# Kernel optimization log

Hardware: AMD Instinct MI355X
Metric: run time of the kernel (lower is better)

The kernel has to match this reference:

```python
import jax, jax.numpy as jnp
import numpy as np

N, L, E = 8, 512, 128
H_DIM = 256            # hidden_dim
Q_DIM = 512            # query_vec dim (config.input_dim, q_update=False)
IN_DIM = 2 * H_DIM     # mean_max tok2ent doubles dim
N_HEADS, N_TYPE = 4, 3
FH = H_DIM // N_HEADS  # per-head out_dim = 64
LSTM_IN, LSTM_H = 2 * H_DIM, H_DIM // 2  # 512 -> 128 per direction
LRELU = 0.2


def lstm_dir(x, Wih, Whh, bih, bhh, reverse):
    # x: (N, L, D); PyTorch gate order i, f, g, o
    if reverse:
        x = jnp.flip(x, axis=1)
    n = x.shape[0]
    def step(carry, xt):
        h, c = carry
        gates = xt @ Wih.T + h @ Whh.T + bih + bhh
        i, f, g, o = jnp.split(gates, 4, axis=-1)
        c = jax.nn.sigmoid(f) * c + jax.nn.sigmoid(i) * jnp.tanh(g)
        h = jax.nn.sigmoid(o) * jnp.tanh(c)
        return (h, c), h
    init = (jnp.zeros((n, LSTM_H), x.dtype), jnp.zeros((n, LSTM_H), x.dtype))
    _, ys = jax.lax.scan(step, init, jnp.swapaxes(x, 0, 1))
    ys = jnp.swapaxes(ys, 0, 1)
    if reverse:
        ys = jnp.flip(ys, axis=1)
    return ys


def setup_inputs():
    key = jax.random.key(0)
    ks = jax.random.split(key, 16)
    s = 0.05
    return {
        'doc_state': jax.random.normal(ks[0], (N, L, H_DIM), jnp.float32),
        'query_vec': jax.random.normal(ks[1], (N, Q_DIM), jnp.float32),
        'context_mask': jnp.ones((N, L), jnp.float32),
        'ent_mapping': (jax.random.uniform(ks[2], (N, E, L)) < 0.03).astype(jnp.float32),
        'ent_mask': jnp.ones((N, E), jnp.float32),
        'query_weight': jax.random.normal(ks[3], (Q_DIM, IN_DIM), jnp.float32) * s,
        'W_type': jax.random.normal(ks[4], (N_HEADS, N_TYPE, IN_DIM, FH), jnp.float32) * s,
        'a_type': jax.random.normal(ks[5], (N_HEADS, N_TYPE, 2 * FH, 1), jnp.float32) * s,
        'qattn_W1': jax.random.normal(ks[6], (N_HEADS, N_TYPE, Q_DIM, 2 * FH), jnp.float32) * s,
        'qattn_W2': jax.random.normal(ks[7], (N_HEADS, N_TYPE, 2 * FH, 2 * FH), jnp.float32) * s,
        'Wih_f': jax.random.normal(ks[8], (4 * LSTM_H, LSTM_IN), jnp.float32) * s,
        'Whh_f': jax.random.normal(ks[9], (4 * LSTM_H, LSTM_H), jnp.float32) * s,
        'bih_f': jnp.zeros((4 * LSTM_H,), jnp.float32),
        'bhh_f': jnp.zeros((4 * LSTM_H,), jnp.float32),
        'Wih_b': jax.random.normal(ks[10], (4 * LSTM_H, LSTM_IN), jnp.float32) * s,
        'Whh_b': jax.random.normal(ks[11], (4 * LSTM_H, LSTM_H), jnp.float32) * s,
        'bih_b': jnp.zeros((4 * LSTM_H,), jnp.float32),
        'bhh_b': jnp.zeros((4 * LSTM_H,), jnp.float32),
        'context_lens': jnp.full((N,), L, jnp.int32),
        'graphs': jax.random.randint(ks[12], (N, E, E), 0, N_TYPE + 1, jnp.int32),
    }


def reference(doc_state, query_vec, context_mask, ent_mapping, ent_mask,
              query_weight, W_type, a_type, qattn_W1, qattn_W2,
              Wih_f, Whh_f, bih_f, bhh_f, Wih_b, Whh_b, bih_b, bhh_b,
              context_lens, graphs):
    adj = graphs  # (N, E, E), values in {0..N_TYPE}
    # --- MeanMaxPooling tok2ent (entity_lens computed as in BasicBlock) ---
    ent_len = ent_mapping.sum(-1)
    ent_len = ent_len + (ent_len == 0)
    es = ent_mapping[:, :, :, None] * doc_state[:, None]          # (N,E,L,d)
    max_p = es.max(axis=2)
    mean_p = es.sum(axis=2) / ent_len[:, :, None]
    entity_state = jnp.concatenate([max_p, mean_p], axis=-1)      # (N,E,2d)
    # --- query-conditioned soft mask ---
    temp = np.float32(np.sqrt(Q_DIM * IN_DIM))
    query = query_vec @ query_weight                              # (N,2d)
    query_scores = jnp.einsum('ned,nd->ne', entity_state, query)[..., None] / temp
    softmask = query_scores * ent_mask[:, :, None]                # (N,E,1)
    adj_mask = jax.nn.sigmoid(softmask)
    # --- multi-head multi-relation GAT (score computed without E^2*2d concat) ---
    h_all = jnp.einsum('ned,htdf->htnef', entity_state, W_type)   # (H,T,N,E,f)
    qg = jax.nn.relu(jnp.einsum('nd,htdg->htng', query_vec, qattn_W1))
    qg = jax.nn.sigmoid(jnp.einsum('htng,htgk->htnk', qg, qattn_W2))  # (H,T,N,2f)
    g1, g2 = qg[..., :FH], qg[..., FH:]
    a = a_type[..., 0]                                            # (H,T,2f)
    a1, a2 = a[..., :FH], a[..., FH:]
    src = jnp.einsum('htnef,htnf,htf->htne', h_all, g1, a1)
    dst = jnp.einsum('htnef,htnf,htf->htne', h_all, g2, a2)
    sc = src[..., :, None] + dst[..., None, :]                    # (H,T,N,E,E)
    sc = jnp.where(sc > 0, sc, LRELU * sc)                        # lrelu:0.2
    type_ids = jnp.arange(1, N_TYPE + 1, dtype=adj.dtype).reshape(1, N_TYPE, 1, 1, 1)
    scores = jnp.sum(jnp.where(adj[None, None] == type_ids, sc, jnp.float32(0)), axis=1)  # (H,N,E,E)
    scores = jnp.where(adj[None] > 0, scores, jnp.float32(-1e30))
    coefs = jax.nn.softmax(scores, axis=-1)
    # original code multiplies the LAST edge-type's h by node_mask, then aggregates
    h_last = h_all[:, -1] * adj_mask[None]                        # (H,N,E,f)
    heads = jnp.einsum('hnij,hnjf->hnif', coefs, h_last)          # (H,N,E,f)
    ent_out = jnp.transpose(heads, (1, 2, 0, 3)).reshape(N, E, H_DIM)
    entity_state2 = jax.nn.relu(ent_out)                          # (N,E,hid)
    # --- InteractionLayer (LSTM branch; all lengths == L so packing is a no-op) ---
    expand = jnp.einsum('ned,nel->nld', entity_state2, ent_mapping)  # (N,L,hid)
    inp = jnp.concatenate([expand, doc_state], axis=-1)           # (N,L,2*hid)
    fwd = lstm_dir(inp, Wih_f, Whh_f, bih_f, bhh_f, False)
    bwd = lstm_dir(inp, Wih_b, Whh_b, bih_b, bhh_b, True)
    doc_out = jnp.concatenate([fwd, bwd], axis=-1)                # (N,L,hid)
    return doc_out, entity_state2, softmask
```

## Files before the change

### kernel.cpp

```cpp
#include <hip/hip_runtime.h>
#include <math.h>

typedef _Float16 h2 __attribute__((ext_vector_type(2)));
typedef _Float16 f16x8 __attribute__((ext_vector_type(8)));
typedef __attribute__((ext_vector_type(8))) short bf16x8;
typedef __attribute__((ext_vector_type(4))) float f32x4;

__device__ __forceinline__ float sigm(float x){ return 1.f/(1.f+expf(-x)); }

__device__ __forceinline__ float fsigm(float x){
  float e = __expf(-x);
  return __builtin_amdgcn_rcpf(1.f + e);
}
__device__ __forceinline__ float ftanh(float x){
  float xx = fminf(fmaxf(x, -15.f), 15.f);
  float e = __expf(2.f * xx);
  return 1.f - 2.f * __builtin_amdgcn_rcpf(e + 1.f);
}
__device__ __forceinline__ h2 u2h(unsigned u){
  union { unsigned u; h2 h; } x; x.u = u; return x.h;
}
template<int CTRL>
__device__ __forceinline__ float qperm(float v){
  return __int_as_float(__builtin_amdgcn_mov_dpp(__float_as_int(v), CTRL, 0xf, 0xf, true));
}
__device__ __forceinline__ unsigned short f2bf(float f){
  union{float f; unsigned u;} x; x.f = f;
  unsigned r = x.u + 0x7FFF + ((x.u >> 16) & 1);
  return (unsigned short)(r >> 16);
}

__global__ void k_ent_state(const float* __restrict__ doc, const float* __restrict__ emap,
                            float* __restrict__ ES, _Float16* __restrict__ ES16){
  int ne = blockIdx.x;
  int n = ne >> 7;
  int tid = threadIdx.x;
  __shared__ int idx_l[512];
  __shared__ int cnt_s;
  if (tid < 64){
    int total = 0;
    for (int base = 0; base < 512; base += 64){
      float m = emap[(size_t)ne*512 + base + tid];
      unsigned long long mask = __ballot(m != 0.f);
      int pos = __popcll(mask & ((1ull << tid) - 1ull));
      if (m != 0.f) idx_l[total + pos] = base + tid;
      total += __popcll(mask);
    }
    if (tid == 0) cnt_s = total;
  }
  __syncthreads();
  int cnt = cnt_s;
  const float* dbase = doc + (size_t)n*512*256 + tid;
  const float* mrow = emap + (size_t)ne*512;
  float sum = 0.f, mx = -3.402823e38f, msum = 0.f;
  for (int i = 0; i < cnt; i++){
    int l = idx_l[i];
    float m = mrow[l];
    float v = m * dbase[(size_t)l*256];
    sum += v; mx = fmaxf(mx, v); msum += m;
  }
  if (cnt < 512) mx = fmaxf(mx, 0.f);
  float elen = (msum == 0.f) ? 1.f : msum;
  float mean = sum / elen;
  float* o = ES + (size_t)ne*512;
  o[tid] = mx;
  o[256 + tid] = mean;
  _Float16* o16 = ES16 + (size_t)ne*512;
  o16[tid] = (_Float16)mx;
  o16[256 + tid] = (_Float16)mean;
}

__global__ __launch_bounds__(256) void k_wtprep(const float* __restrict__ Wt,
                                                _Float16* __restrict__ WtT){
  int kt = blockIdx.x;
  int ht = blockIdx.y;
  int tid = threadIdx.x;
  __shared__ _Float16 tile[64][65];
  for (int rep = 0; rep < 16; rep++){
    int linear = rep*256 + tid;
    int k = linear >> 6, f = linear & 63;
    tile[f][k] = (_Float16)Wt[((size_t)ht*512 + kt*64 + k)*64 + f];
  }
  __syncthreads();
  for (int rep = 0; rep < 16; rep++){
    int linear = rep*256 + tid;
    int f = linear >> 6, k = linear & 63;
    WtT[((size_t)ht*64 + f)*512 + kt*64 + k] = tile[f][k];
  }
}

__global__ __launch_bounds__(256) void k_colidx(const float* __restrict__ emap,
                                                int* __restrict__ cidx, int* __restrict__ ccnt){
  int lt = blockIdx.x;
  int n = blockIdx.y;
  int l0 = lt*32;
  int tid = threadIdx.x;
  __shared__ float tile[128][33];
  int l = tid & 31, eg = tid >> 5;
  for (int i = 0; i < 16; i++){
    int e = eg*16 + i;
    tile[e][l] = emap[((size_t)n*128 + e)*512 + l0 + l];
  }
  __syncthreads();
  if (tid < 32){
    int ll = tid;
    int b = n*512 + l0 + ll;
    int* out = cidx + (size_t)b*128;
    int cnt = 0;
    for (int e = 0; e < 128; e++){
      if (tile[e][ll] != 0.f) out[cnt++] = e;
    }
    ccnt[b] = cnt;
  }
}

__global__ __launch_bounds__(256) void k_query2(const float* __restrict__ qv,
                                                const float* __restrict__ qw,
                                                float* __restrict__ Q){
  int b = blockIdx.x;
  int n = b >> 3, ct = b & 7;
  int tid = threadIdx.x;
  int col = ct*64 + (tid & 63), ks = tid >> 6;
  const float* qvp = qv + n*512 + ks*128;
  const float* qwp = qw + (size_t)(ks*128)*512 + col;
  float acc = 0.f;
  for (int k = 0; k < 128; k++) acc += qvp[k] * qwp[(size_t)k*512];
  __shared__ float part[4][64];
  part[ks][tid & 63] = acc;
  __syncthreads();
  if (tid < 64)
    Q[n*512 + ct*64 + tid] = part[0][tid] + part[1][tid] + part[2][tid] + part[3][tid];
}

__global__ __launch_bounds__(64) void k_qscore2(const float* __restrict__ ES,
                         const float* __restrict__ Q, const float* __restrict__ emask,
                         float* __restrict__ sm_out, float* __restrict__ AM){
  int ne = blockIdx.x;
  int n = ne >> 7;
  int lane = threadIdx.x;
  const float* es = ES + (size_t)ne*512;
  const float* q = Q + n*512;
  float a = 0.f;
  for (int k = lane; k < 512; k += 64) a += es[k] * q[k];
  #pragma unroll
  for (int o = 32; o > 0; o >>= 1) a += __shfl_xor(a, o, 64);
  if (lane == 0){
    float s = (a * (1.f/512.f)) * emask[ne];
    sm_out[ne] = s;
    AM[ne] = sigm(s);
  }
}

__global__ __launch_bounds__(256) void k_hall(const _Float16* __restrict__ ES16,
                                              const _Float16* __restrict__ WtT,
                                              float* __restrict__ HALL){
  int net = blockIdx.x;
  int ht  = blockIdx.y;
  int tid = threadIdx.x;
  int lane = tid & 63, w = tid >> 6;
  int wm = w >> 1, wg = w & 1;
  int m0 = net*64 + wm*32;
  int f0 = wg*32;
  int lr = lane & 15, lk8 = (lane >> 4) * 8;

  const _Float16* a0p = ES16 + (size_t)(m0 + lr)*512 + lk8;
  const _Float16* a1p = a0p + (size_t)16*512;
  const _Float16* b0p = WtT + ((size_t)ht*64 + f0 + lr)*512 + lk8;
  const _Float16* b1p = b0p + (size_t)16*512;

  f32x4 acc[2][2] = {};
  for (int k0 = 0; k0 < 512; k0 += 32){
    f16x8 af[2], bfr[2];
    af[0] = *(const f16x8*)a0p;
    af[1] = *(const f16x8*)a1p;
    bfr[0] = *(const f16x8*)b0p;
    bfr[1] = *(const f16x8*)b1p;
    a0p += 32; a1p += 32; b0p += 32; b1p += 32;
    #pragma unroll
    for (int im = 0; im < 2; im++)
      #pragma unroll
      for (int ig = 0; ig < 2; ig++)
        acc[im][ig] = __builtin_amdgcn_mfma_f32_16x16x32_f16(af[im], bfr[ig], acc[im][ig], 0, 0, 0);
  }
  int crow = (lane >> 4) * 4;
  int ccol = lane & 15;
  #pragma unroll
  for (int im = 0; im < 2; im++)
    #pragma unroll
    for (int ig = 0; ig < 2; ig++){
      int f = f0 + ig*16 + ccol;
      #pragma unroll
      for (int r = 0; r < 4; r++){
        int m = m0 + im*16 + crow + r;
        HALL[((size_t)ht*1024 + m)*64 + f] = acc[im][ig][r];
      }
    }
}

__global__ __launch_bounds__(256) void k_qattn(const float* __restrict__ qv,
                        const float* __restrict__ W1, const float* __restrict__ W2,
                        const float* __restrict__ at, float* __restrict__ WSRC,
                        float* __restrict__ WDST){
  int b = blockIdx.x;
  int ht = b >> 3, n = b & 7;
  int tid = threadIdx.x;
  int f = tid & 127, kh = tid >> 7;
  __shared__ float qv_s[512];
  __shared__ float part[2][128];
  __shared__ float qg1[128];
  for (int i = tid; i < 512; i += 256) qv_s[i] = qv[n*512 + i];
  __syncthreads();
  const float* w1 = W1 + (size_t)ht*512*128 + (size_t)kh*256*128 + f;
  float acc = 0.f;
  for (int k = 0; k < 256; k++) acc += qv_s[kh*256 + k] * w1[(size_t)k*128];
  part[kh][f] = acc;
  __syncthreads();
  if (kh == 0) qg1[f] = fmaxf(part[0][f] + part[1][f], 0.f);
  __syncthreads();
  const float* w2 = W2 + (size_t)ht*128*128 + (size_t)kh*64*128 + f;
  float acc2 = 0.f;
  for (int g = 0; g < 64; g++) acc2 += qg1[kh*64 + g] * w2[(size_t)g*128];
  part[kh][f] = acc2;
  __syncthreads();
  if (kh == 0){
    float coef = sigm(part[0][f] + part[1][f]) * at[ht*128 + f];
    if (f < 64) WSRC[(ht*8 + n)*64 + f] = coef;
    else        WDST[(ht*8 + n)*64 + f - 64] = coef;
  }
}

__global__ void k_srcdst(const float* __restrict__ HALL, const float* __restrict__ WSRC,
                         const float* __restrict__ WDST, float* __restrict__ SRC,
                         float* __restrict__ DST){
  int b = blockIdx.x;
  int e = threadIdx.x;
  __shared__ float w1[64], w2[64];
  if (e < 64) w1[e] = WSRC[b*64 + e]; else w2[e-64] = WDST[b*64 + e - 64];
  __syncthreads();
  int ht = b >> 3, n = b & 7;
  const float* h = HALL + ((size_t)ht*1024 + n*128 + e)*64;
  float s = 0.f, d = 0.f;
  #pragma unroll 8
  for (int f = 0; f < 64; f++){ float hv = h[f]; s += hv*w1[f]; d += hv*w2[f]; }
  SRC[b*128 + e] = s; DST[b*128 + e] = d;
}

__global__ void k_attn(const float* __restrict__ HALL, const float* __restrict__ SRC,
                       const float* __restrict__ DST, const float* __restrict__ AM,
                       const int* __restrict__ adj, float* __restrict__ ES2,
                       float* __restrict__ out_ent){
  int b = blockIdx.x;
  int h = b >> 6, n = (b >> 3) & 7, chunk = b & 7;
  int i0 = chunk*16;
  int tid = threadIdx.x;
  __shared__ float dst_l[3][128];
  __shared__ float src_l[3][16];
  __shared__ float hl[128][65];
  __shared__ float coef_l[128];
  __shared__ float redbuf[2];
  __shared__ float part2[2][64];
  for (int idx = tid; idx < 384; idx += 128){
    int t = idx >> 7, j = idx & 127;
    dst_l[t][j] = DST[((h*3 + t)*8 + n)*128 + j];
  }
  if (tid < 48){
    int t = tid >> 4, r = tid & 15;
    src_l[t][r] = SRC[((h*3 + t)*8 + n)*128 + i0 + r];
  }
  for (int idx = tid; idx < 8192; idx += 128){
    int j = idx >> 6, f = idx & 63;
    hl[j][f] = HALL[((size_t)(h*3 + 2)*1024 + n*128 + j)*64 + f] * AM[n*128 + j];
  }
  __syncthreads();
  const int* arow = adj + (size_t)n*128*128;
  int w = tid >> 6, f = tid & 63;
  for (int r = 0; r < 16; r++){
    int i = i0 + r;
    int a = arow[(size_t)i*128 + tid];
    float s;
    if (a > 0){
      float v = src_l[a-1][r] + dst_l[a-1][tid];
      s = v > 0.f ? v : 0.2f*v;
    } else s = -1e30f;
    float m = s;
    #pragma unroll
    for (int o = 32; o > 0; o >>= 1) m = fmaxf(m, __shfl_xor(m, o, 64));
    if ((tid & 63) == 0) redbuf[w] = m;
    __syncthreads();
    float mx = fmaxf(redbuf[0], redbuf[1]);
    float p = expf(s - mx);
    float ps = p;
    #pragma unroll
    for (int o = 32; o > 0; o >>= 1) ps += __shfl_xor(ps, o, 64);
    __syncthreads();
    if ((tid & 63) == 0) redbuf[w] = ps;
    __syncthreads();
    float denom = redbuf[0] + redbuf[1];
    coef_l[tid] = p / denom;
    __syncthreads();
    float acc = 0.f;
    for (int jj = 0; jj < 64; jj++) acc += coef_l[w*64 + jj] * hl[w*64 + jj][f];
    part2[w][f] = acc;
    __syncthreads();
    if (tid < 64){
      float v = fmaxf(part2[0][tid] + part2[1][tid], 0.f);
      size_t oidx = ((size_t)n*128 + i)*256 + h*64 + tid;
      ES2[oidx] = v;
      out_ent[oidx] = v;
    }
    __syncthreads();
  }
}

__global__ void k_expand(const float* __restrict__ ES2, const float* __restrict__ emap,
                         const float* __restrict__ doc, const int* __restrict__ cidx,
                         const int* __restrict__ ccnt, float* __restrict__ INP){
  int b = blockIdx.x;
  int n = b >> 9, l = b & 511;
  int tid = threadIdx.x;
  int cnt = ccnt[b];
  const int* idx = cidx + (size_t)b*128;
  float acc = 0.f;
  const float* e2 = ES2 + (size_t)n*128*256 + tid;
  for (int i = 0; i < cnt; i++){
    int e = idx[i];
    float m = emap[((size_t)n*128 + e)*512 + l];
    acc += m * e2[(size_t)e*256];
  }
  float* o = INP + (size_t)b*512;
  o[tid] = acc;
  o[256 + tid] = doc[(size_t)b*256 + tid];
}

__global__ __launch_bounds__(256) void k_gatein(const float* __restrict__ INP,
                         const float* __restrict__ Wf, const float* __restrict__ Wb,
                         const float* __restrict__ bihf, const float* __restrict__ bhhf,
                         const float* __restrict__ bihb, const float* __restrict__ bhhb,
                         float* __restrict__ GF, float* __restrict__ GB){
  int mt = blockIdx.x, gt = blockIdx.y, dir = blockIdx.z;
  const float* W = dir ? Wb : Wf;
  float* Gout = dir ? GB : GF;
  const float* bi = dir ? bihb : bihf;
  const float* bh = dir ? bhhb : bhhf;
  int tid = threadIdx.x;
  int lane = tid & 63, w = tid >> 6;
  int wm = w >> 1, wg = w & 1;
  int m0 = mt*64 + wm*32;
  int g0 = gt*64 + wg*32;
  int lr = lane & 15, lk8 = (lane >> 4) * 8;

  const float* a0p = INP + (size_t)(m0 + lr)*512 + lk8;
  const float* a1p = a0p + (size_t)16*512;
  const float* b0p = W   + (size_t)(g0 + lr)*512 + lk8;
  const float* b1p = b0p + (size_t)16*512;

  f32x4 acc[2][2] = {};
  for (int k0 = 0; k0 < 512; k0 += 32){
    bf16x8 af[2], bfr[2];
    {
      float4 u = *(const float4*)a0p, v = *(const float4*)(a0p + 4);
      bf16x8 r; r[0]=(short)f2bf(u.x); r[1]=(short)f2bf(u.y); r[2]=(short)f2bf(u.z); r[3]=(short)f2bf(u.w);
      r[4]=(short)f2bf(v.x); r[5]=(short)f2bf(v.y); r[6]=(short)f2bf(v.z); r[7]=(short)f2bf(v.w);
      af[0]=r;
    }
    {
      float4 u = *(const float4*)a1p, v = *(const float4*)(a1p + 4);
      bf16x8 r; r[0]=(short)f2bf(u.x); r[1]=(short)f2bf(u.y); r[2]=(short)f2bf(u.z); r[3]=(short)f2bf(u.w);
      r[4]=(short)f2bf(v.x); r[5]=(short)f2bf(v.y); r[6]=(short)f2bf(v.z); r[7]=(short)f2bf(v.w);
      af[1]=r;
    }
    {
      float4 u = *(const float4*)b0p, v = *(const float4*)(b0p + 4);
      bf16x8 r; r[0]=(short)f2bf(u.x); r[1]=(short)f2bf(u.y); r[2]=(short)f2bf(u.z); r[3]=(short)f2bf(u.w);
      r[4]=(short)f2bf(v.x); r[5]=(short)f2bf(v.y); r[6]=(short)f2bf(v.z); r[7]=(short)f2bf(v.w);
      bfr[0]=r;
    }
    {
      float4 u = *(const float4*)b1p, v = *(const float4*)(b1p + 4);
      bf16x8 r; r[0]=(short)f2bf(u.x); r[1]=(short)f2bf(u.y); r[2]=(short)f2bf(u.z); r[3]=(short)f2bf(u.w);
      r[4]=(short)f2bf(v.x); r[5]=(short)f2bf(v.y); r[6]=(short)f2bf(v.z); r[7]=(short)f2bf(v.w);
      bfr[1]=r;
    }
    a0p += 32; a1p += 32; b0p += 32; b1p += 32;
    #pragma unroll
    for (int im = 0; im < 2; im++)
      #pragma unroll
      for (int ig = 0; ig < 2; ig++)
        acc[im][ig] = __builtin_amdgcn_mfma_f32_16x16x32_bf16(af[im], bfr[ig], acc[im][ig], 0, 0, 0);
  }
  int crow = (lane >> 4) * 4;
  int ccol = lane & 15;
  #pragma unroll
  for (int im = 0; im < 2; im++)
    #pragma unroll
    for (int ig = 0; ig < 2; ig++){
      int g = g0 + ig*16 + ccol;
      float bias = bi[g] + bh[g];
      int p = (g & 127)*4 + (g >> 7);
      #pragma unroll
      for (int r = 0; r < 4; r++){
        int m = m0 + im*16 + crow + r;
        Gout[(size_t)m*512 + p] = acc[im][ig][r] + bias;
      }
    }
}

__global__ __launch_bounds__(256) void k_lstm(const float* __restrict__ GF,
                                              const float* __restrict__ GB,
                                              const float* __restrict__ Whhf,
                                              const float* __restrict__ Whhb,
                                              float* __restrict__ out){
  int b = blockIdx.x;
  int dir = b >> 3, n = b & 7;
  const float* G = dir ? GB : GF;
  const float* Whh = dir ? Whhb : Whhf;
  int tid = threadIdx.x;
  int j = tid >> 1;
  int s = tid & 1;

  h2 wreg[4][32];
  #pragma unroll
  for (int q = 0; q < 4; q++){
    const float* wp = Whh + (size_t)(q*128 + j)*128 + 64*s;
    #pragma unroll
    for (int kk = 0; kk < 32; kk++){
      h2 p; p[0] = (_Float16)wp[2*kk]; p[1] = (_Float16)wp[2*kk+1];
      wreg[q][kk] = p;
    }
  }

  __shared__ __align__(16) _Float16 h_l[2][128];
  if (tid < 128) h_l[0][tid] = (_Float16)0.f;

  const float4* Gp = (const float4*)(G + (size_t)n*512*512) + (dir ? (size_t)511*128 : 0) + j;
  const int gstep = dir ? -128 : 128;
  float* outp = out + (size_t)n*512*256 + (dir ? (size_t)511*256 : 0) + dir*128 + j;
  const int ostep = dir ? -256 : 256;

  float4 ga, gb, gc, gd;
  ga = *Gp; Gp += gstep;
  gb = *Gp; Gp += gstep;
  gc = *Gp; Gp += gstep;
  gd = *Gp; Gp += gstep;
  float c = 0.f;
  __syncthreads();

#define LSTM_STEP(RB, GREG)                                                    \
  {                                                                            \
    const uint4* hb = (const uint4*)(&h_l[RB][64*s]);                          \
    uint4 hv[8];                                                               \
    _Pragma("unroll")                                                          \
    for (int r = 0; r < 8; r++) hv[r] = hb[r];                                 \
    float gci = GREG.x, gcf = GREG.y, gcg = GREG.z, gco = GREG.w;              \
    GREG = *Gp; Gp += gstep;                                                   \
    float accf[4];                                                             \
    _Pragma("unroll")                                                          \
    for (int q = 0; q < 4; q++){                                               \
      h2 a0; a0[0]=(_Float16)0.f; a0[1]=(_Float16)0.f; h2 a1 = a0;             \
      _Pragma("unroll")                                                        \
      for (int r = 0; r < 8; r++){                                             \
        a0 += wreg[q][4*r+0] * u2h(hv[r].x);                                   \
        a1 += wreg[q][4*r+1] * u2h(hv[r].y);                                   \
        a0 += wreg[q][4*r+2] * u2h(hv[r].z);                                   \
        a1 += wreg[q][4*r+3] * u2h(hv[r].w);                                   \
      }                                                                        \
      h2 hs = a0 + a1;                                                         \
      accf[q] = (float)hs[0] + (float)hs[1];                                   \
    }                                                                          \
    _Pragma("unroll")                                                          \
    for (int q = 0; q < 4; q++){                                               \
      accf[q] += qperm<0xB1>(accf[q]);                                         \
    }                                                                          \
    float vi = accf[0] + gci, vf = accf[1] + gcf;                              \
    float vg = accf[2] + gcg, vo = accf[3] + gco;                              \
    c = fsigm(vf) * c + fsigm(vi) * ftanh(vg);                                 \
    float hval = fsigm(vo) * ftanh(c);                                         \
    if (s == 0) h_l[RB^1][j] = (_Float16)hval;                                 \
    else        *outp = hval;                                                  \
    outp += ostep;                                                             \
    asm volatile("s_waitcnt lgkmcnt(0)\n\ts_barrier" ::: "memory");            \
  }

  for (int t = 0; t < 512; t += 4){
    LSTM_STEP(0, ga)
    LSTM_STEP(1, gb)
    LSTM_STEP(0, gc)
    LSTM_STEP(1, gd)
  }
#undef LSTM_STEP
}

extern "C" void kernel_launch(void* const* d_in, const int* in_sizes, int n_in,
                              void* d_out, int out_size, void* d_ws, size_t ws_size,
                              hipStream_t stream){
  const float* doc   = (const float*)d_in[0];
  const float* qvec  = (const float*)d_in[1];
  const float* emap  = (const float*)d_in[3];
  const float* emask = (const float*)d_in[4];
  const float* qw    = (const float*)d_in[5];
  const float* Wt    = (const float*)d_in[6];
  const float* at    = (const float*)d_in[7];
  const float* qa1   = (const float*)d_in[8];
  const float* qa2   = (const float*)d_in[9];
  const float* Wihf  = (const float*)d_in[10];
  const float* Whhf  = (const float*)d_in[11];
  const float* bihf  = (const float*)d_in[12];
  const float* bhhf  = (const float*)d_in[13];
  const float* Wihb  = (const float*)d_in[14];
  const float* Whhb  = (const float*)d_in[15];
  const float* bihb  = (const float*)d_in[16];
  const float* bhhb  = (const float*)d_in[17];
  const int*   adj   = (const int*)d_in[19];

  float* out = (float*)d_out;
  float* out_doc = out;
  float* out_ent = out + 8*512*256;
  float* out_sm  = out_ent + 8*128*256;

  float* w = (float*)d_ws;
  float* ES   = w; w += 8*128*512;
  float* AM   = w; w += 8*128;
  float* Q    = w; w += 8*512;
  float* HALL = w; w += 12*1024*64;
  float* WSRC = w; w += 12*8*64;
  float* WDST = w; w += 12*8*64;
  float* SRC  = w; w += 12*8*128;
  float* DST  = w; w += 12*8*128;
  float* ES2  = w; w += 8*128*256;
  float* INP  = w; w += 8*512*512;
  float* GF   = w; w += 8*512*512;
  w += 4096;
  float* GB   = w; w += 8*512*512;
  w += 4096;
  _Float16* ES16 = (_Float16*)w; w += 8*128*512/2;
  _Float16* WtT  = (_Float16*)w; w += 12*64*512/2;
  int* cidx = (int*)w; w += 4096*128;
  int* ccnt = (int*)w; w += 4096;

  hipLaunchKernelGGL(k_colidx,    dim3(16,8), dim3(256), 0, stream, emap, cidx, ccnt);
  hipLaunchKernelGGL(k_wtprep,    dim3(8,12), dim3(256), 0, stream, Wt, WtT);
  hipLaunchKernelGGL(k_ent_state, dim3(1024), dim3(256), 0, stream, doc, emap, ES, ES16);
  hipLaunchKernelGGL(k_query2,    dim3(64),   dim3(256), 0, stream, qvec, qw, Q);
  hipLaunchKernelGGL(k_qscore2,   dim3(1024), dim3(64),  0, stream, ES, Q, emask, out_sm, AM);
  hipLaunchKernelGGL(k_hall,      dim3(16,12),dim3(256), 0, stream, ES16, WtT, HALL);
  hipLaunchKernelGGL(k_qattn,     dim3(96),   dim3(256), 0, stream, qvec, qa1, qa2, at, WSRC, WDST);
  hipLaunchKernelGGL(k_srcdst,    dim3(96),   dim3(128), 0, stream, HALL, WSRC, WDST, SRC, DST);
  hipLaunchKernelGGL(k_attn,      dim3(256),  dim3(128), 0, stream, HALL, SRC, DST, AM, adj, ES2, out_ent);
  hipLaunchKernelGGL(k_expand,    dim3(4096), dim3(256), 0, stream, ES2, emap, doc, cidx, ccnt, INP);
  hipLaunchKernelGGL(k_gatein,    dim3(64,8,2), dim3(256), 0, stream, INP, Wihf, Wihb, bihf, bhhf, bihb, bhhb, GF, GB);
  hipLaunchKernelGGL(k_lstm,      dim3(16),   dim3(256), 0, stream, GF, GB, Whhf, Whhb, out_doc);
}
```

Before: 421.0 us.

## Batch LSTM recurrence across sequences with MFMA in one block per direction

The recurrent LSTM kernel changes from one block per (direction, batch) doing packed-half dot products to one 512-thread block per direction. That block computes the hidden-to-gate product for all 8 sequences at once with 16x16x32 f16 MFMA instructions, padding the batch to 16 columns. A new prep kernel writes Whh into fp16 in MFMA A-fragment layout so the weights load straight into registers. This cuts per-step ALU work but puts each direction on a single CU and wastes half the MFMA columns on padding. Latency per step now depends on the MFMA chain plus the transcendental math.

```diff
diff --git a/kernel.cpp b/kernel.cpp
--- a/kernel.cpp
+++ b/kernel.cpp
@@ -16,13 +16,6 @@
   float xx = fminf(fmaxf(x, -15.f), 15.f);
   float e = __expf(2.f * xx);
   return 1.f - 2.f * __builtin_amdgcn_rcpf(e + 1.f);
-}
-__device__ __forceinline__ h2 u2h(unsigned u){
-  union { unsigned u; h2 h; } x; x.u = u; return x.h;
-}
-template<int CTRL>
-__device__ __forceinline__ float qperm(float v){
-  return __int_as_float(__builtin_amdgcn_mov_dpp(__float_as_int(v), CTRL, 0xf, 0xf, true));
 }
 __device__ __forceinline__ unsigned short f2bf(float f){
   union{float f; unsigned u;} x; x.f = f;
@@ -89,6 +82,25 @@
   }
 }
 
+__global__ __launch_bounds__(256) void k_whhprep(const float* __restrict__ Whhf,
+                                                 const float* __restrict__ Whhb,
+                                                 _Float16* __restrict__ WA){
+  int dir = blockIdx.y;
+  const float* Whh = dir ? Whhb : Whhf;
+  _Float16* outb = WA + (size_t)dir*512*128;
+  int slot = blockIdx.x*256 + threadIdx.x;
+  int l = slot & 63;
+  int tile = slot >> 6;
+  int kc = tile & 3, mt = (tile >> 2) & 3, wv = tile >> 4;
+  int lane_lo = l & 15, khi = l >> 4;
+  int girow = wv*64 + mt*16 + lane_lo;
+  int j = girow >> 2, q = girow & 3;
+  const float* src = Whh + (size_t)(q*128 + j)*128 + kc*32 + khi*8;
+  _Float16* dst = outb + (size_t)slot*8;
+  #pragma unroll
+  for (int i = 0; i < 8; i++) dst[i] = (_Float16)src[i];
+}
+
 __global__ __launch_bounds__(256) void k_colidx(const float* __restrict__ emap,
                                                 int* __restrict__ cidx, int* __restrict__ ccnt){
   int lt = blockIdx.x;
@@ -105,10 +117,10 @@
   if (tid < 32){
     int ll = tid;
     int b = n*512 + l0 + ll;
-    int* out = cidx + (size_t)b*128;
+    int* outp = cidx + (size_t)b*128;
     int cnt = 0;
     for (int e = 0; e < 128; e++){
-      if (tile[e][ll] != 0.f) out[cnt++] = e;
+      if (tile[e][ll] != 0.f) outp[cnt++] = e;
     }
     ccnt[b] = cnt;
   }
@@ -405,87 +417,85 @@
     }
 }
 
-__global__ __launch_bounds__(256) void k_lstm(const float* __restrict__ GF,
+__global__ __launch_bounds__(512) void k_lstm(const float* __restrict__ GF,
                                               const float* __restrict__ GB,
-                                              const float* __restrict__ Whhf,
-                                              const float* __restrict__ Whhb,
+                                              const _Float16* __restrict__ WA,
                                               float* __restrict__ out){
-  int b = blockIdx.x;
-  int dir = b >> 3, n = b & 7;
+  int dir = blockIdx.x;
   const float* G = dir ? GB : GF;
-  const float* Whh = dir ? Whhb : Whhf;
-  int tid = threadIdx.x;
-  int j = tid >> 1;
-  int s = tid & 1;
-
-  h2 wreg[4][32];
-  #pragma unroll
-  for (int q = 0; q < 4; q++){
-    const float* wp = Whh + (size_t)(q*128 + j)*128 + 64*s;
-    #pragma unroll
-    for (int kk = 0; kk < 32; kk++){
-      h2 p; p[0] = (_Float16)wp[2*kk]; p[1] = (_Float16)wp[2*kk+1];
-      wreg[q][kk] = p;
-    }
-  }
-
-  __shared__ __align__(16) _Float16 h_l[2][128];
-  if (tid < 128) h_l[0][tid] = (_Float16)0.f;
-
-  const float4* Gp = (const float4*)(G + (size_t)n*512*512) + (dir ? (size_t)511*128 : 0) + j;
-  const int gstep = dir ? -128 : 128;
-  float* outp = out + (size_t)n*512*256 + (dir ? (size_t)511*256 : 0) + dir*128 + j;
-  const int ostep = dir ? -256 : 256;
-
-  float4 ga, gb, gc, gd;
-  ga = *Gp; Gp += gstep;
-  gb = *Gp; Gp += gstep;
-  gc = *Gp; Gp += gstep;
-  gd = *Gp; Gp += gstep;
-  float c = 0.f;
+  const _Float16* wa = WA + (size_t)dir*512*128;
+  int tid = threadIdx.x;
+  int lane = tid & 63, wv = tid >> 6;
+  int n = lane & 15;
+  int nc = n & 7;
+  int uhi = lane >> 4;
+  bool active = (n < 8);
+
+  f16x8 afrag[4][4];
+  #pragma unroll
+  for (int mt = 0; mt < 4; mt++)
+    #pragma unroll
+    for (int kc = 0; kc < 4; kc++){
+      int slot = ((wv*4 + mt)*4 + kc)*64 + lane;
+      afrag[mt][kc] = *(const f16x8*)(wa + (size_t)slot*8);
+    }
+
+  __shared__ __align__(16) _Float16 h_lds[2][16][136];
+  for (int i = tid; i < 2*16*136; i += 512) ((_Float16*)h_lds)[i] = (_Float16)0.f;
+
+  int j0 = 16*wv + uhi;
+  int tt0 = dir ? 511 : 0;
+  const float* Gp = G + (size_t)(nc*512 + tt0)*512 + 4*j0;
+  const long gstep = dir ? -512 : 512;
+  float* outp = out + (size_t)(nc*512 + tt0)*256 + dir*128 + j0;
+  const long ostep = dir ? -256 : 256;
+
+  float4 gA[4], gB[4];
+  #pragma unroll
+  for (int mt = 0; mt < 4; mt++) gA[mt] = *(const float4*)(Gp + mt*16);
+  Gp += gstep;
+  #pragma unroll
+  for (int mt = 0; mt < 4; mt++) gB[mt] = *(const float4*)(Gp + mt*16);
+  Gp += gstep;
+
+  float cst[4] = {0.f, 0.f, 0.f, 0.f};
   __syncthreads();
 
 #define LSTM_STEP(RB, GREG)                                                    \
   {                                                                            \
-    const uint4* hb = (const uint4*)(&h_l[RB][64*s]);                          \
-    uint4 hv[8];                                                               \
+    const _Float16* hrow = &h_lds[RB][n][0];                                   \
+    f16x8 bfrag[4];                                                            \
     _Pragma("unroll")                                                          \
-    for (int r = 0; r < 8; r++) hv[r] = hb[r];                                 \
-    float gci = GREG.x, gcf = GREG.y, gcg = GREG.z, gco = GREG.w;              \
-    GREG = *Gp; Gp += gstep;                                                   \
-    float accf[4];                                                             \
+    for (int kc = 0; kc < 4; kc++)                                             \
+      bfrag[kc] = *(const f16x8*)(hrow + kc*32 + uhi*8);                       \
+    f32x4 acc[4] = {};                                                         \
     _Pragma("unroll")                                                          \
-    for (int q = 0; q < 4; q++){                                               \
-      h2 a0; a0[0]=(_Float16)0.f; a0[1]=(_Float16)0.f; h2 a1 = a0;             \
+    for (int mt = 0; mt < 4; mt++)                                             \
       _Pragma("unroll")                                                        \
-      for (int r = 0; r < 8; r++){                                             \
-        a0 += wreg[q][4*r+0] * u2h(hv[r].x);                                   \
-        a1 += wreg[q][4*r+1] * u2h(hv[r].y);                                   \
-        a0 += wreg[q][4*r+2] * u2h(hv[r].z);                                   \
-        a1 += wreg[q][4*r+3] * u2h(hv[r].w);                                   \
+      for (int kc = 0; kc < 4; kc++)                                           \
+        acc[mt] = __builtin_amdgcn_mfma_f32_16x16x32_f16(afrag[mt][kc],        \
+                      bfrag[kc], acc[mt], 0, 0, 0);                            \
+    _Pragma("unroll")                                                          \
+    for (int mt = 0; mt < 4; mt++){                                            \
+      float4 g = GREG[mt];                                                     \
+      GREG[mt] = *(const float4*)(Gp + mt*16);                                 \
+      float vi = acc[mt][0] + g.x, vf = acc[mt][1] + g.y;                      \
+      float vg = acc[mt][2] + g.z, vo = acc[mt][3] + g.w;                      \
+      cst[mt] = fsigm(vf)*cst[mt] + fsigm(vi)*ftanh(vg);                       \
+      float hval = fsigm(vo)*ftanh(cst[mt]);                                   \
+      if (active){                                                             \
+        h_lds[RB^1][n][j0 + 4*mt] = (_Float16)hval;                            \
+        outp[4*mt] = hval;                                                     \
       }                                                                        \
-      h2 hs = a0 + a1;                                                         \
-      accf[q] = (float)hs[0] + (float)hs[1];                                   \
     }                                                                          \
-    _Pragma("unroll")                                                          \
-    for (int q = 0; q < 4; q++){                                               \
-      accf[q] += qperm<0xB1>(accf[q]);                                         \
-    }                                                                          \
-    float vi = accf[0] + gci, vf = accf[1] + gcf;                              \
-    float vg = accf[2] + gcg, vo = accf[3] + gco;                              \
-    c = fsigm(vf) * c + fsigm(vi) * ftanh(vg);                                 \
-    float hval = fsigm(vo) * ftanh(c);                                         \
-    if (s == 0) h_l[RB^1][j] = (_Float16)hval;                                 \
-    else        *outp = hval;                                                  \
+    Gp += gstep;                                                               \
     outp += ostep;                                                             \
     asm volatile("s_waitcnt lgkmcnt(0)\n\ts_barrier" ::: "memory");            \
   }
 
-  for (int t = 0; t < 512; t += 4){
-    LSTM_STEP(0, ga)
-    LSTM_STEP(1, gb)
-    LSTM_STEP(0, gc)
-    LSTM_STEP(1, gd)
+  for (int t = 0; t < 512; t += 2){
+    LSTM_STEP(0, gA)
+    LSTM_STEP(1, gB)
   }
 #undef LSTM_STEP
 }
@@ -534,11 +544,13 @@
   w += 4096;
   _Float16* ES16 = (_Float16*)w; w += 8*128*512/2;
   _Float16* WtT  = (_Float16*)w; w += 12*64*512/2;
+  _Float16* WA   = (_Float16*)w; w += 2*512*128/2;
   int* cidx = (int*)w; w += 4096*128;
   int* ccnt = (int*)w; w += 4096;
 
   hipLaunchKernelGGL(k_colidx,    dim3(16,8), dim3(256), 0, stream, emap, cidx, ccnt);
   hipLaunchKernelGGL(k_wtprep,    dim3(8,12), dim3(256), 0, stream, Wt, WtT);
+  hipLaunchKernelGGL(k_whhprep,   dim3(32,2), dim3(256), 0, stream, Whhf, Whhb, WA);
   hipLaunchKernelGGL(k_ent_state, dim3(1024), dim3(256), 0, stream, doc, emap, ES, ES16);
   hipLaunchKernelGGL(k_query2,    dim3(64),   dim3(256), 0, stream, qvec, qw, Q);
   hipLaunchKernelGGL(k_qscore2,   dim3(1024), dim3(64),  0, stream, ES, Q, emask, out_sm, AM);
@@ -548,5 +560,5 @@
   hipLaunchKernelGGL(k_attn,      dim3(256),  dim3(128), 0, stream, HALL, SRC, DST, AM, adj, ES2, out_ent);
   hipLaunchKernelGGL(k_expand,    dim3(4096), dim3(256), 0, stream, ES2, emap, doc, cidx, ccnt, INP);
   hipLaunchKernelGGL(k_gatein,    dim3(64,8,2), dim3(256), 0, stream, INP, Wihf, Wihb, bihf, bhhf, bihb, bhhb, GF, GB);
-  hipLaunchKernelGGL(k_lstm,      dim3(16),   dim3(256), 0, stream, GF, GB, Whhf, Whhb, out_doc);
-}
+  hipLaunchKernelGGL(k_lstm,      dim3(2),    dim3(512), 0, stream, GF, GB, WA, out_doc);
+}
```

Measured after the change: 699.5 us. 1.66x slower.

## Merge independent prologue kernels into two block-dispatched megakernels

Applied to the files above, without the earlier changes.

Combines colidx, wtprep, ent_state, query and qattn into one kernel that picks its role from the block index, and combines qscore and the HALL MFMA GEMM into a second one. Qscore now packs four entities per 256-thread block. This cuts launches from twelve to seven and lets independent work run concurrently, aiming to remove launch gaps and tail idle time. The cost is a larger shared-memory footprint and register allocation set by the heaviest branch, which may lower occupancy for the lighter roles.

```diff
diff --git a/kernel.cpp b/kernel.cpp
--- a/kernel.cpp
+++ b/kernel.cpp
@@ -30,202 +30,195 @@
   return (unsigned short)(r >> 16);
 }
 
-__global__ void k_ent_state(const float* __restrict__ doc, const float* __restrict__ emap,
-                            float* __restrict__ ES, _Float16* __restrict__ ES16){
-  int ne = blockIdx.x;
-  int n = ne >> 7;
+__global__ __launch_bounds__(256) void k_mega1(
+    const float* __restrict__ doc, const float* __restrict__ emap,
+    const float* __restrict__ qv, const float* __restrict__ qw,
+    const float* __restrict__ Wt, const float* __restrict__ W1,
+    const float* __restrict__ W2, const float* __restrict__ at,
+    int* __restrict__ cidx, int* __restrict__ ccnt,
+    _Float16* __restrict__ WtT, float* __restrict__ ES,
+    _Float16* __restrict__ ES16, float* __restrict__ Q,
+    float* __restrict__ WSRC, float* __restrict__ WDST){
+  __shared__ __align__(16) char smem[16896];
+  int b = blockIdx.x;
   int tid = threadIdx.x;
-  __shared__ int idx_l[512];
-  __shared__ int cnt_s;
-  if (tid < 64){
-    int total = 0;
-    for (int base = 0; base < 512; base += 64){
-      float m = emap[(size_t)ne*512 + base + tid];
-      unsigned long long mask = __ballot(m != 0.f);
-      int pos = __popcll(mask & ((1ull << tid) - 1ull));
-      if (m != 0.f) idx_l[total + pos] = base + tid;
-      total += __popcll(mask);
-    }
-    if (tid == 0) cnt_s = total;
-  }
-  __syncthreads();
-  int cnt = cnt_s;
-  const float* dbase = doc + (size_t)n*512*256 + tid;
-  const float* mrow = emap + (size_t)ne*512;
-  float sum = 0.f, mx = -3.402823e38f, msum = 0.f;
-  for (int i = 0; i < cnt; i++){
-    int l = idx_l[i];
-    float m = mrow[l];
-    float v = m * dbase[(size_t)l*256];
-    sum += v; mx = fmaxf(mx, v); msum += m;
-  }
-  if (cnt < 512) mx = fmaxf(mx, 0.f);
-  float elen = (msum == 0.f) ? 1.f : msum;
-  float mean = sum / elen;
-  float* o = ES + (size_t)ne*512;
-  o[tid] = mx;
-  o[256 + tid] = mean;
-  _Float16* o16 = ES16 + (size_t)ne*512;
-  o16[tid] = (_Float16)mx;
-  o16[256 + tid] = (_Float16)mean;
-}
-
-__global__ __launch_bounds__(256) void k_wtprep(const float* __restrict__ Wt,
-                                                _Float16* __restrict__ WtT){
-  int kt = blockIdx.x;
-  int ht = blockIdx.y;
+
+  if (b < 128){
+    float (*tile)[33] = (float(*)[33])smem;
+    int lt = b & 15, n = b >> 4;
+    int l0 = lt*32;
+    int l = tid & 31, eg = tid >> 5;
+    for (int i = 0; i < 16; i++){
+      int e = eg*16 + i;
+      tile[e][l] = emap[((size_t)n*128 + e)*512 + l0 + l];
+    }
+    __syncthreads();
+    if (tid < 32){
+      int ll = tid;
+      int bb = n*512 + l0 + ll;
+      int* outp = cidx + (size_t)bb*128;
+      int cnt = 0;
+      for (int e = 0; e < 128; e++){
+        if (tile[e][ll] != 0.f) outp[cnt++] = e;
+      }
+      ccnt[bb] = cnt;
+    }
+  } else if (b < 224){
+    _Float16 (*tile)[65] = (_Float16(*)[65])smem;
+    int rb = b - 128;
+    int kt = rb & 7, ht = rb >> 3;
+    for (int rep = 0; rep < 16; rep++){
+      int linear = rep*256 + tid;
+      int k = linear >> 6, f = linear & 63;
+      tile[f][k] = (_Float16)Wt[((size_t)ht*512 + kt*64 + k)*64 + f];
+    }
+    __syncthreads();
+    for (int rep = 0; rep < 16; rep++){
+      int linear = rep*256 + tid;
+      int f = linear >> 6, k = linear & 63;
+      WtT[((size_t)ht*64 + f)*512 + kt*64 + k] = tile[f][k];
+    }
+  } else if (b < 1248){
+    int* idx_l = (int*)smem;
+    int* cnt_p = (int*)(smem + 2048);
+    int ne = b - 224;
+    int n = ne >> 7;
+    if (tid < 64){
+      int total = 0;
+      for (int base = 0; base < 512; base += 64){
+        float m = emap[(size_t)ne*512 + base + tid];
+        unsigned long long mask = __ballot(m != 0.f);
+        int pos = __popcll(mask & ((1ull << tid) - 1ull));
+        if (m != 0.f) idx_l[total + pos] = base + tid;
+        total += __popcll(mask);
+      }
+      if (tid == 0) *cnt_p = total;
+    }
+    __syncthreads();
+    int cnt = *cnt_p;
+    const float* dbase = doc + (size_t)n*512*256 + tid;
+    const float* mrow = emap + (size_t)ne*512;
+    float sum = 0.f, mx = -3.402823e38f, msum = 0.f;
+    for (int i = 0; i < cnt; i++){
+      int l = idx_l[i];
+      float m = mrow[l];
+      float v = m * dbase[(size_t)l*256];
+      sum += v; mx = fmaxf(mx, v); msum += m;
+    }
+    if (cnt < 512) mx = fmaxf(mx, 0.f);
+    float elen = (msum == 0.f) ? 1.f : msum;
+    float mean = sum / elen;
+    float* o = ES + (size_t)ne*512;
+    o[tid] = mx;
+    o[256 + tid] = mean;
+    _Float16* o16 = ES16 + (size_t)ne*512;
+    o16[tid] = (_Float16)mx;
+    o16[256 + tid] = (_Float16)mean;
+  } else if (b < 1312){
+    float (*part)[64] = (float(*)[64])smem;
+    int rb = b - 1248;
+    int n = rb >> 3, ct = rb & 7;
+    int col = ct*64 + (tid & 63), ks = tid >> 6;
+    const float* qvp = qv + n*512 + ks*128;
+    const float* qwp = qw + (size_t)(ks*128)*512 + col;
+    float acc = 0.f;
+    for (int k = 0; k < 128; k++) acc += qvp[k] * qwp[(size_t)k*512];
+    part[ks][tid & 63] = acc;
+    __syncthreads();
+    if (tid < 64)
+      Q[n*512 + ct*64 + tid] = part[0][tid] + part[1][tid] + part[2][tid] + part[3][tid];
+  } else {
+    float* qv_s = (float*)smem;
+    float* partb = qv_s + 512;
+    float* qg1 = partb + 256;
+    int rb = b - 1312;
+    int ht = rb >> 3, n = rb & 7;
+    int f = tid & 127, kh = tid >> 7;
+    for (int i = tid; i < 512; i += 256) qv_s[i] = qv[n*512 + i];
+    __syncthreads();
+    const float* w1 = W1 + (size_t)ht*512*128 + (size_t)kh*256*128 + f;
+    float acc = 0.f;
+    for (int k = 0; k < 256; k++) acc += qv_s[kh*256 + k] * w1[(size_t)k*128];
+    partb[kh*128 + f] = acc;
+    __syncthreads();
+    if (kh == 0) qg1[f] = fmaxf(partb[f] + partb[128 + f], 0.f);
+    __syncthreads();
+    const float* w2 = W2 + (size_t)ht*128*128 + (size_t)kh*64*128 + f;
+    float acc2 = 0.f;
+    for (int g = 0; g < 64; g++) acc2 += qg1[kh*64 + g] * w2[(size_t)g*128];
+    partb[kh*128 + f] = acc2;
+    __syncthreads();
+    if (kh == 0){
+      float coef = sigm(partb[f] + partb[128 + f]) * at[ht*128 + f];
+      if (f < 64) WSRC[(ht*8 + n)*64 + f] = coef;
+      else        WDST[(ht*8 + n)*64 + f - 64] = coef;
+    }
+  }
+}
+
+__global__ __launch_bounds__(256) void k_mega2(
+    const float* __restrict__ ES, const float* __restrict__ Q,
+    const float* __restrict__ emask, const _Float16* __restrict__ ES16,
+    const _Float16* __restrict__ WtT, float* __restrict__ sm_out,
+    float* __restrict__ AM, float* __restrict__ HALL){
+  int b = blockIdx.x;
   int tid = threadIdx.x;
-  __shared__ _Float16 tile[64][65];
-  for (int rep = 0; rep < 16; rep++){
-    int linear = rep*256 + tid;
-    int k = linear >> 6, f = linear & 63;
-    tile[f][k] = (_Float16)Wt[((size_t)ht*512 + kt*64 + k)*64 + f];
-  }
-  __syncthreads();
-  for (int rep = 0; rep < 16; rep++){
-    int linear = rep*256 + tid;
-    int f = linear >> 6, k = linear & 63;
-    WtT[((size_t)ht*64 + f)*512 + kt*64 + k] = tile[f][k];
-  }
-}
-
-__global__ __launch_bounds__(256) void k_colidx(const float* __restrict__ emap,
-                                                int* __restrict__ cidx, int* __restrict__ ccnt){
-  int lt = blockIdx.x;
-  int n = blockIdx.y;
-  int l0 = lt*32;
-  int tid = threadIdx.x;
-  __shared__ float tile[128][33];
-  int l = tid & 31, eg = tid >> 5;
-  for (int i = 0; i < 16; i++){
-    int e = eg*16 + i;
-    tile[e][l] = emap[((size_t)n*128 + e)*512 + l0 + l];
-  }
-  __syncthreads();
-  if (tid < 32){
-    int ll = tid;
-    int b = n*512 + l0 + ll;
-    int* out = cidx + (size_t)b*128;
-    int cnt = 0;
-    for (int e = 0; e < 128; e++){
-      if (tile[e][ll] != 0.f) out[cnt++] = e;
-    }
-    ccnt[b] = cnt;
-  }
-}
-
-__global__ __launch_bounds__(256) void k_query2(const float* __restrict__ qv,
-                                                const float* __restrict__ qw,
-                                                float* __restrict__ Q){
-  int b = blockIdx.x;
-  int n = b >> 3, ct = b & 7;
-  int tid = threadIdx.x;
-  int col = ct*64 + (tid & 63), ks = tid >> 6;
-  const float* qvp = qv + n*512 + ks*128;
-  const float* qwp = qw + (size_t)(ks*128)*512 + col;
-  float acc = 0.f;
-  for (int k = 0; k < 128; k++) acc += qvp[k] * qwp[(size_t)k*512];
-  __shared__ float part[4][64];
-  part[ks][tid & 63] = acc;
-  __syncthreads();
-  if (tid < 64)
-    Q[n*512 + ct*64 + tid] = part[0][tid] + part[1][tid] + part[2][tid] + part[3][tid];
-}
-
-__global__ __launch_bounds__(64) void k_qscore2(const float* __restrict__ ES,
-                         const float* __restrict__ Q, const float* __restrict__ emask,
-                         float* __restrict__ sm_out, float* __restrict__ AM){
-  int ne = blockIdx.x;
-  int n = ne >> 7;
-  int lane = threadIdx.x;
-  const float* es = ES + (size_t)ne*512;
-  const float* q = Q + n*512;
-  float a = 0.f;
-  for (int k = lane; k < 512; k += 64) a += es[k] * q[k];
-  #pragma unroll
-  for (int o = 32; o > 0; o >>= 1) a += __shfl_xor(a, o, 64);
-  if (lane == 0){
-    float s = (a * (1.f/512.f)) * emask[ne];
-    sm_out[ne] = s;
-    AM[ne] = sigm(s);
-  }
-}
-
-__global__ __launch_bounds__(256) void k_hall(const _Float16* __restrict__ ES16,
-                                              const _Float16* __restrict__ WtT,
-                                              float* __restrict__ HALL){
-  int net = blockIdx.x;
-  int ht  = blockIdx.y;
-  int tid = threadIdx.x;
-  int lane = tid & 63, w = tid >> 6;
-  int wm = w >> 1, wg = w & 1;
-  int m0 = net*64 + wm*32;
-  int f0 = wg*32;
-  int lr = lane & 15, lk8 = (lane >> 4) * 8;
-
-  const _Float16* a0p = ES16 + (size_t)(m0 + lr)*512 + lk8;
-  const _Float16* a1p = a0p + (size_t)16*512;
-  const _Float16* b0p = WtT + ((size_t)ht*64 + f0 + lr)*512 + lk8;
-  const _Float16* b1p = b0p + (size_t)16*512;
-
-  f32x4 acc[2][2] = {};
-  for (int k0 = 0; k0 < 512; k0 += 32){
-    f16x8 af[2], bfr[2];
-    af[0] = *(const f16x8*)a0p;
-    af[1] = *(const f16x8*)a1p;
-    bfr[0] = *(const f16x8*)b0p;
-    bfr[1] = *(const f16x8*)b1p;
-    a0p += 32; a1p += 32; b0p += 32; b1p += 32;
+  if (b < 256){
+    int wv = tid >> 6, lane = tid & 63;
+    int ne = b*4 + wv;
+    int n = ne >> 7;
+    const float* es = ES + (size_t)ne*512;
+    const float* q = Q + n*512;
+    float a = 0.f;
+    for (int k = lane; k < 512; k += 64) a += es[k] * q[k];
+    #pragma unroll
+    for (int o = 32; o > 0; o >>= 1) a += __shfl_xor(a, o, 64);
+    if (lane == 0){
+      float s = (a * (1.f/512.f)) * emask[ne];
+      sm_out[ne] = s;
+      AM[ne] = sigm(s);
+    }
+  } else {
+    int idx = b - 256;
+    int net = idx & 15, ht = idx >> 4;
+    int lane = tid & 63, w = tid >> 6;
+    int wm = w >> 1, wg = w & 1;
+    int m0 = net*64 + wm*32;
+    int f0 = wg*32;
+    int lr = lane & 15, lk8 = (lane >> 4) * 8;
+
+    const _Float16* a0p = ES16 + (size_t)(m0 + lr)*512 + lk8;
+    const _Float16* a1p = a0p + (size_t)16*512;
+    const _Float16* b0p = WtT + ((size_t)ht*64 + f0 + lr)*512 + lk8;
+    const _Float16* b1p = b0p + (size_t)16*512;
+
+    f32x4 acc[2][2] = {};
+    for (int k0 = 0; k0 < 512; k0 += 32){
+      f16x8 af[2], bfr[2];
+      af[0] = *(const f16x8*)a0p;
+      af[1] = *(const f16x8*)a1p;
+      bfr[0] = *(const f16x8*)b0p;
+      bfr[1] = *(const f16x8*)b1p;
+      a0p += 32; a1p += 32; b0p += 32; b1p += 32;
+      #pragma unroll
+      for (int im = 0; im < 2; im++)
+        #pragma unroll
+        for (int ig = 0; ig < 2; ig++)
+          acc[im][ig] = __builtin_amdgcn_mfma_f32_16x16x32_f16(af[im], bfr[ig], acc[im][ig], 0, 0, 0);
+    }
+    int crow = (lane >> 4) * 4;
+    int ccol = lane & 15;
     #pragma unroll
     for (int im = 0; im < 2; im++)
       #pragma unroll
-      for (int ig = 0; ig < 2; ig++)
-        acc[im][ig] = __builtin_amdgcn_mfma_f32_16x16x32_f16(af[im], bfr[ig], acc[im][ig], 0, 0, 0);
-  }
-  int crow = (lane >> 4) * 4;
-  int ccol = lane & 15;
-  #pragma unroll
-  for (int im = 0; im < 2; im++)
-    #pragma unroll
-    for (int ig = 0; ig < 2; ig++){
-      int f = f0 + ig*16 + ccol;
-      #pragma unroll
-      for (int r = 0; r < 4; r++){
-        int m = m0 + im*16 + crow + r;
-        HALL[((size_t)ht*1024 + m)*64 + f] = acc[im][ig][r];
+      for (int ig = 0; ig < 2; ig++){
+        int f = f0 + ig*16 + ccol;
+        #pragma unroll
+        for (int r = 0; r < 4; r++){
+          int m = m0 + im*16 + crow + r;
+          HALL[((size_t)ht*1024 + m)*64 + f] = acc[im][ig][r];
+        }
       }
-    }
-}
-
-__global__ __launch_bounds__(256) void k_qattn(const float* __restrict__ qv,
-                        const float* __restrict__ W1, const float* __restrict__ W2,
-                        const float* __restrict__ at, float* __restrict__ WSRC,
-                        float* __restrict__ WDST){
-  int b = blockIdx.x;
-  int ht = b >> 3, n = b & 7;
-  int tid = threadIdx.x;
-  int f = tid & 127, kh = tid >> 7;
-  __shared__ float qv_s[512];
-  __shared__ float part[2][128];
-  __shared__ float qg1[128];
-  for (int i = tid; i < 512; i += 256) qv_s[i] = qv[n*512 + i];
-  __syncthreads();
-  const float* w1 = W1 + (size_t)ht*512*128 + (size_t)kh*256*128 + f;
-  float acc = 0.f;
-  for (int k = 0; k < 256; k++) acc += qv_s[kh*256 + k] * w1[(size_t)k*128];
-  part[kh][f] = acc;
-  __syncthreads();
-  if (kh == 0) qg1[f] = fmaxf(part[0][f] + part[1][f], 0.f);
-  __syncthreads();
-  const float* w2 = W2 + (size_t)ht*128*128 + (size_t)kh*64*128 + f;
-  float acc2 = 0.f;
-  for (int g = 0; g < 64; g++) acc2 += qg1[kh*64 + g] * w2[(size_t)g*128];
-  part[kh][f] = acc2;
-  __syncthreads();
-  if (kh == 0){
-    float coef = sigm(part[0][f] + part[1][f]) * at[ht*128 + f];
-    if (f < 64) WSRC[(ht*8 + n)*64 + f] = coef;
-    else        WDST[(ht*8 + n)*64 + f - 64] = coef;
   }
 }
 
@@ -537,16 +530,14 @@
   int* cidx = (int*)w; w += 4096*128;
   int* ccnt = (int*)w; w += 4096;
 
-  hipLaunchKernelGGL(k_colidx,    dim3(16,8), dim3(256), 0, stream, emap, cidx, ccnt);
-  hipLaunchKernelGGL(k_wtprep,    dim3(8,12), dim3(256), 0, stream, Wt, WtT);
-  hipLaunchKernelGGL(k_ent_state, dim3(1024), dim3(256), 0, stream, doc, emap, ES, ES16);
-  hipLaunchKernelGGL(k_query2,    dim3(64),   dim3(256), 0, stream, qvec, qw, Q);
-  hipLaunchKernelGGL(k_qscore2,   dim3(1024), dim3(64),  0, stream, ES, Q, emask, out_sm, AM);
-  hipLaunchKernelGGL(k_hall,      dim3(16,12),dim3(256), 0, stream, ES16, WtT, HALL);
-  hipLaunchKernelGGL(k_qattn,     dim3(96),   dim3(256), 0, stream, qvec, qa1, qa2, at, WSRC, WDST);
-  hipLaunchKernelGGL(k_srcdst,    dim3(96),   dim3(128), 0, stream, HALL, WSRC, WDST, SRC, DST);
-  hipLaunchKernelGGL(k_attn,      dim3(256),  dim3(128), 0, stream, HALL, SRC, DST, AM, adj, ES2, out_ent);
-  hipLaunchKernelGGL(k_expand,    dim3(4096), dim3(256), 0, stream, ES2, emap, doc, cidx, ccnt, INP);
-  hipLaunchKernelGGL(k_gatein,    dim3(64,8,2), dim3(256), 0, stream, INP, Wihf, Wihb, bihf, bhhf, bihb, bhhb, GF, GB);
-  hipLaunchKernelGGL(k_lstm,      dim3(16),   dim3(256), 0, stream, GF, GB, Whhf, Whhb, out_doc);
-}
+  hipLaunchKernelGGL(k_mega1,  dim3(1408), dim3(256), 0, stream,
+                     doc, emap, qvec, qw, Wt, qa1, qa2, at,
+                     cidx, ccnt, WtT, ES, ES16, Q, WSRC, WDST);
+  hipLaunchKernelGGL(k_mega2,  dim3(448),  dim3(256), 0, stream,
+                     ES, Q, emask, ES16, WtT, out_sm, AM, HALL);
+  hipLaunchKernelGGL(k_srcdst, dim3(96),   dim3(128), 0, stream, HALL, WSRC, WDST, SRC, DST);
+  hipLaunchKernelGGL(k_attn,   dim3(256),  dim3(128), 0, stream, HALL, SRC, DST, AM, adj, ES2, out_ent);
+  hipLaunchKernelGGL(k_expand, dim3(4096), dim3(256), 0, stream, ES2, emap, doc, cidx, ccnt, INP);
+  hipLaunchKernelGGL(k_gatein, dim3(64,8,2), dim3(256), 0, stream, INP, Wihf, Wihb, bihf, bhhf, bihb, bhhb, GF, GB);
+  hipLaunchKernelGGL(k_lstm,   dim3(16),   dim3(256), 0, stream, GF, GB, Whhf, Whhb, out_doc);
+}
```

After: 394.3 us. -6.3%, faster.
